# Performance work log

Hardware: AMD Instinct MI355X
Metric: run time of the kernel (lower is better)

## Reference

```python
import jax, jax.numpy as jnp
import numpy as np

N_AGENTS, OBS_DIM, HID, ACT_DIM = 8192, 64, 128, 16


def setup_inputs() -> dict:
    key = jax.random.key(0)
    k = jax.random.split(key, 8)
    obs_agents = jax.random.normal(k[0], (N_AGENTS, OBS_DIM), dtype=jnp.float32)
    # binary adjacency, {0,1}, int32 (index/mask semantics, non-differentiable)
    adj = jax.random.randint(k[1], (N_AGENTS, N_AGENTS), 0, 2, dtype=jnp.int32)
    def lin(kk, fan_in, fan_out):
        lim = 1.0 / np.sqrt(fan_in)
        kw, kb = jax.random.split(kk)
        W = jax.random.uniform(kw, (fan_in, fan_out), jnp.float32, -lim, lim)
        b = jax.random.uniform(kb, (fan_out,), jnp.float32, -lim, lim)
        return W, b
    W1, b1 = lin(k[2], OBS_DIM, HID)          # encoder
    W2, b2 = lin(k[3], 2 * HID, HID)          # actor layer 1
    W3, b3 = lin(k[4], HID, ACT_DIM)          # actor layer 2
    return {"obs_agents": obs_agents, "adj": adj,
            "W1": W1, "b1": b1, "W2": W2, "b2": b2, "W3": W3, "b3": b3}


def reference(obs_agents, adj, W1, b1, W2, b2, W3, b3):
    # per-agent encode: h = tanh(obs @ W1 + b1)  -> [N, HID]
    h = jnp.tanh(obs_agents @ W1 + b1)
    # neighbor mean message: mean of h[j] over j with adj[i,j]!=0, zeros if no neighbors
    a = adj.astype(h.dtype)                      # [N, N] binary
    deg = jnp.sum(a, axis=1, keepdims=True)      # [N, 1]
    msg = (a @ h) / jnp.maximum(deg, 1.0)        # zero rows stay zero
    # actor MLP on concat([h, msg])
    combined = jnp.concatenate([h, msg], axis=-1)            # [N, 2*HID]
    hid = jnp.tanh(combined @ W2 + b2)                        # [N, HID]
    logits = hid @ W3 + b3                                    # [N, ACT_DIM]
    return logits
```

## Files before the change

kernel.cpp:

```cpp
#include <hip/hip_runtime.h>
#include <stdint.h>
#include <math.h>

#define NAG 8192
#define NC  128
#define NSPLIT 8
#define LDB2 136

typedef __attribute__((ext_vector_type(8))) short short8;
typedef __attribute__((ext_vector_type(4))) float floatx4;

__device__ __forceinline__ float bf2f(unsigned short u) {
    union { uint32_t i; float f; } v; v.i = ((uint32_t)u) << 16; return v.f;
}
__device__ __forceinline__ unsigned short f2bf(float f) {
    union { float f; uint32_t i; } v; v.f = f;
    uint32_t x = v.i;
    return (unsigned short)((x + 0x7FFFu + ((x >> 16) & 1u)) >> 16);
}
__device__ __forceinline__ unsigned short f2h(float f) {
    union { _Float16 h; unsigned short u; } v; v.h = (_Float16)f; return v.u;
}
__device__ __forceinline__ float h2f(unsigned short u) {
    union { _Float16 h; unsigned short u; } v; v.u = u; return (float)v.h;
}
__device__ __forceinline__ bool detect_f32(const void* W1, int t) {
    const unsigned short* w = (const unsigned short*)W1;
    int l = t & 63, big = 0;
    #pragma unroll
    for (int j = 0; j < 8; ++j) {
        float v = bf2f(w[l * 8 + j]);
        if (!(fabsf(v) <= 1e6f)) big = 1;
    }
    return __ballot(big) != 0ull;
}

__global__ __launch_bounds__(256) void kA_pack_encode(
    const int* __restrict__ adj,
    unsigned long long* __restrict__ bits,
    const void* __restrict__ obs,
    const void* __restrict__ W1,
    const void* __restrict__ b1,
    float* __restrict__ h_f32,
    unsigned short* __restrict__ hT)
{
    const int t = threadIdx.x;
    if (blockIdx.x < 2048) {
        const int lane = t & 63;
        const int gw = blockIdx.x * 4 + (t >> 6);
        for (int it = 0; it < 32; ++it) {
            size_t u = ((size_t)it * 8192 + gw) * 4;
            size_t col = u * 64 + lane;
            unsigned long long m0 = __ballot(adj[col]       != 0);
            unsigned long long m1 = __ballot(adj[col + 64]  != 0);
            unsigned long long m2 = __ballot(adj[col + 128] != 0);
            unsigned long long m3 = __ballot(adj[col + 192] != 0);
            if (lane == 0) {
                bits[u]     = m0;
                bits[u + 1] = m1;
                bits[u + 2] = m2;
                bits[u + 3] = m3;
            }
        }
        return;
    }
    __shared__ float obs_lds[32][68];
    __shared__ unsigned short ht_lds[128][33];
    const int abase = (blockIdx.x - 2048) * 32;
    const bool isf = detect_f32(W1, t);

    {
        int a = t >> 3, c0 = (t & 7) * 8;
        if (isf) {
            const float* p = (const float*)obs;
            #pragma unroll
            for (int j = 0; j < 8; ++j)
                obs_lds[a][c0 + j] = p[(size_t)(abase + a) * 64 + c0 + j];
        } else {
            const unsigned short* p = (const unsigned short*)obs;
            #pragma unroll
            for (int j = 0; j < 8; ++j)
                obs_lds[a][c0 + j] = bf2f(p[(size_t)(abase + a) * 64 + c0 + j]);
        }
    }
    __syncthreads();

    const int o = t & 127;
    const int half = t >> 7;
    float acc[16];
    if (isf) {
        const float* Wp = (const float*)W1;
        float bias = ((const float*)b1)[o];
        #pragma unroll
        for (int i = 0; i < 16; ++i) acc[i] = bias;
        for (int k0 = 0; k0 < 64; k0 += 8) {
            float w[8];
            #pragma unroll
            for (int j = 0; j < 8; ++j) w[j] = Wp[(k0 + j) * 128 + o];
            #pragma unroll
            for (int j = 0; j < 8; ++j)
                #pragma unroll
                for (int i = 0; i < 16; ++i)
                    acc[i] = fmaf(obs_lds[half * 16 + i][k0 + j], w[j], acc[i]);
        }
    } else {
        const unsigned short* Wp = (const unsigned short*)W1;
        float bias = bf2f(((const unsigned short*)b1)[o]);
        #pragma unroll
        for (int i = 0; i < 16; ++i) acc[i] = bias;
        for (int k0 = 0; k0 < 64; k0 += 8) {
            float w[8];
            #pragma unroll
            for (int j = 0; j < 8; ++j) w[j] = bf2f(Wp[(k0 + j) * 128 + o]);
            #pragma unroll
            for (int j = 0; j < 8; ++j)
                #pragma unroll
                for (int i = 0; i < 16; ++i)
                    acc[i] = fmaf(obs_lds[half * 16 + i][k0 + j], w[j], acc[i]);
        }
    }
    #pragma unroll
    for (int i = 0; i < 16; ++i) {
        float th = tanhf(acc[i]);
        int a = half * 16 + i;
        h_f32[(size_t)(abase + a) * 128 + o] = th;
        ht_lds[o][a] = f2bf(th);
    }
    __syncthreads();

    for (int p = 0; p < 16; ++p) {
        int n = p * 8 + (t >> 5);
        int a = t & 31;
        hT[(size_t)n * NAG + abase + a] = ht_lds[n][a];
    }
}

__global__ __launch_bounds__(256, 4) void k2_msggemm(
    const uint32_t* __restrict__ bits,
    const unsigned short* __restrict__ hT,
    unsigned short* __restrict__ Cp16)
{
    __shared__ __align__(16) unsigned short Blds[128 * LDB2];
    const int t = threadIdx.x;
    const int mtile = blockIdx.x & 127;
    const int ks = blockIdx.x >> 7;
    const int row0 = mtile * 64;
    const int kbeg = ks * 1024;

    const int wave = t >> 6, lane = t & 63;
    const int fm = lane & 15, quad = lane >> 4;

    floatx4 acc[8];
    #pragma unroll
    for (int i = 0; i < 8; ++i) acc[i] = (floatx4)0.f;

    const int arow = row0 + wave * 16 + fm;
    const uint32_t* aWp = bits + (size_t)arow * 256 + (kbeg >> 5);

    for (int ss = 0; ss < 8; ++ss) {
        if (ss) __syncthreads();
        #pragma unroll
        for (int i = 0; i < 8; ++i) {
            int idx = i * 256 + t;
            int row = idx >> 4, ch = idx & 15;
            uint4 v = *reinterpret_cast<const uint4*>(hT + (size_t)row * NAG + kbeg + ss * 128 + ch * 8);
            *reinterpret_cast<uint4*>(&Blds[row * LDB2 + ch * 8]) = v;
        }
        int4 a0 = *reinterpret_cast<const int4*>(aWp + ss * 4);
        uint32_t aw[4] = {(uint32_t)a0.x, (uint32_t)a0.y, (uint32_t)a0.z, (uint32_t)a0.w};
        __syncthreads();
        #pragma unroll
        for (int kw = 0; kw < 4; ++kw) {
            uint32_t b = (aw[kw] >> (quad * 8)) & 0xFFu;
            union { uint32_t u[4]; short8 s; } af;
            #pragma unroll
            for (int p = 0; p < 4; ++p) {
                uint32_t bb = b >> (2 * p);
                af.u[p] = ((bb & 1u) | ((bb & 2u) << 15)) * 0x3F80u;
            }
            #pragma unroll
            for (int j = 0; j < 8; ++j) {
                short8 bf = *reinterpret_cast<const short8*>(&Blds[(j * 16 + fm) * LDB2 + kw * 32 + quad * 8]);
                acc[j] = __builtin_amdgcn_mfma_f32_16x16x32_bf16(af.s, bf, acc[j], 0, 0, 0);
            }
        }
    }

    unsigned short* out = Cp16 + (size_t)ks * (NAG * NC);
    #pragma unroll
    for (int j = 0; j < 8; ++j) {
        int col = j * 16 + fm;
        #pragma unroll
        for (int r = 0; r < 4; ++r) {
            int row = row0 + wave * 16 + quad * 4 + r;
            out[(size_t)row * NC + col] = f2h(acc[j][r]);
        }
    }
}

__global__ __launch_bounds__(256) void k3_actor(
    const float* __restrict__ h_f32,
    const unsigned short* __restrict__ Cp16,
    const unsigned long long* __restrict__ bits,
    const void* __restrict__ W1,
    const void* __restrict__ W2,
    const void* __restrict__ b2,
    const void* __restrict__ W3,
    const void* __restrict__ b3,
    void* __restrict__ out)
{
    __shared__ float4 comb4[8][66];
    __shared__ float hid[8][132];
    __shared__ int degp[8][33];
    __shared__ float inv_lds[8];
    const int t = threadIdx.x;
    const int abase = blockIdx.x * 8;
    const bool isf = detect_f32(W1, t);
    const size_t PS = (size_t)NAG * NC;

    {
        int a = t >> 5, j = t & 31;
        const unsigned long long* bp = bits + (size_t)(abase + a) * 128 + j * 4;
        degp[a][j] = __popcll(bp[0]) + __popcll(bp[1]) + __popcll(bp[2]) + __popcll(bp[3]);
    }
    __syncthreads();
    if (t < 8) {
        int d = 0;
        #pragma unroll
        for (int j = 0; j < 32; ++j) d += degp[t][j];
        inv_lds[t] = 1.0f / fmaxf((float)d, 1.0f);
    }
    __syncthreads();

    #pragma unroll
    for (int jj = 0; jj < 2; ++jj) {
        int idx = jj * 256 + t;
        int a = idx >> 6, q = idx & 63;
        float4 v;
        if (q < 32) {
            v = *reinterpret_cast<const float4*>(h_f32 + (size_t)(abase + a) * 128 + q * 4);
        } else {
            int f = (q - 32) * 4;
            float s0 = 0.f, s1 = 0.f, s2 = 0.f, s3 = 0.f;
            #pragma unroll
            for (int s = 0; s < NSPLIT; ++s) {
                ushort4 p = *reinterpret_cast<const ushort4*>(Cp16 + s * PS + (size_t)(abase + a) * NC + f);
                s0 += h2f(p.x); s1 += h2f(p.y); s2 += h2f(p.z); s3 += h2f(p.w);
            }
            float sc = inv_lds[a];
            v = make_float4(s0 * sc, s1 * sc, s2 * sc, s3 * sc);
        }
        comb4[a][q] = v;
    }
    __syncthreads();

    const int o = t & 127, half = t >> 7;
    float acc[4];
    if (isf) {
        const float* Wp = (const float*)W2;
        float bias = ((const float*)b2)[o];
        #pragma unroll
        for (int i = 0; i < 4; ++i) acc[i] = bias;
        for (int cq = 0; cq < 64; ++cq) {
            float w0 = Wp[(cq * 4 + 0) * 128 + o];
            float w1 = Wp[(cq * 4 + 1) * 128 + o];
            float w2 = Wp[(cq * 4 + 2) * 128 + o];
            float w3 = Wp[(cq * 4 + 3) * 128 + o];
            #pragma unroll
            for (int i = 0; i < 4; ++i) {
                float4 v = comb4[half * 4 + i][cq];
                acc[i] = fmaf(v.x, w0, acc[i]);
                acc[i] = fmaf(v.y, w1, acc[i]);
                acc[i] = fmaf(v.z, w2, acc[i]);
                acc[i] = fmaf(v.w, w3, acc[i]);
            }
        }
    } else {
        const unsigned short* Wp = (const unsigned short*)W2;
        float bias = bf2f(((const unsigned short*)b2)[o]);
        #pragma unroll
        for (int i = 0; i < 4; ++i) acc[i] = bias;
        for (int cq = 0; cq < 64; ++cq) {
            float w0 = bf2f(Wp[(cq * 4 + 0) * 128 + o]);
            float w1 = bf2f(Wp[(cq * 4 + 1) * 128 + o]);
            float w2 = bf2f(Wp[(cq * 4 + 2) * 128 + o]);
            float w3 = bf2f(Wp[(cq * 4 + 3) * 128 + o]);
            #pragma unroll
            for (int i = 0; i < 4; ++i) {
                float4 v = comb4[half * 4 + i][cq];
                acc[i] = fmaf(v.x, w0, acc[i]);
                acc[i] = fmaf(v.y, w1, acc[i]);
                acc[i] = fmaf(v.z, w2, acc[i]);
                acc[i] = fmaf(v.w, w3, acc[i]);
            }
        }
    }
    #pragma unroll
    for (int i = 0; i < 4; ++i)
        hid[half * 4 + i][o] = tanhf(acc[i]);
    __syncthreads();

    if (t < 128) {
        const int q = t & 15, ar = t >> 4;
        float l;
        if (isf) {
            const float* Wp = (const float*)W3;
            l = ((const float*)b3)[q];
            #pragma unroll 4
            for (int oo = 0; oo < 128; ++oo)
                l = fmaf(hid[ar][oo], Wp[oo * 16 + q], l);
        } else {
            const unsigned short* Wp = (const unsigned short*)W3;
            l = bf2f(((const unsigned short*)b3)[q]);
            #pragma unroll 4
            for (int oo = 0; oo < 128; ++oo)
                l = fmaf(hid[ar][oo], bf2f(Wp[oo * 16 + q]), l);
        }
        size_t i0 = (size_t)(abase + ar) * 16 + q;
        if (isf) ((float*)out)[i0] = l;
        else     ((unsigned short*)out)[i0] = f2bf(l);
    }
}

extern "C" void kernel_launch(void* const* d_in, const int* in_sizes, int n_in,
                              void* d_out, int out_size, void* d_ws, size_t ws_size,
                              hipStream_t stream) {
    const void* obs = d_in[0];
    const int*  adj = (const int*)d_in[1];
    const void* W1  = d_in[2];
    const void* b1  = d_in[3];
    const void* W2  = d_in[4];
    const void* b2  = d_in[5];
    const void* W3  = d_in[6];
    const void* b3  = d_in[7];

    char* ws = (char*)d_ws;
    unsigned short* hT   = (unsigned short*)(ws);
    float*          h_f32= (float*)(ws + 2097152);
    unsigned short* Cp16 = (unsigned short*)(ws + 6291456);
    unsigned long long* bits = (unsigned long long*)(ws + 23068672);

    hipLaunchKernelGGL(kA_pack_encode, dim3(2304), dim3(256), 0, stream,
                       adj, bits, obs, W1, b1, h_f32, hT);
    hipLaunchKernelGGL(k2_msggemm, dim3(1024), dim3(256), 0, stream,
                       (const uint32_t*)bits, hT, Cp16);
    hipLaunchKernelGGL(k3_actor, dim3(1024), dim3(256), 0, stream,
                       h_f32, Cp16, bits, W1, W2, b2, W3, b3, d_out);
}
```

Baseline: 432.1 us.

## Read int32 adjacency directly in message GEMM, drop bit-packing pass

Removes the separate pass that packed the int32 adjacency matrix into bitmasks. The message GEMM now loads adj rows directly, converts nonzeros to bf16 ones for the MFMA A operand, and accumulates per-row degree partials written per K-split. The actor kernel sums these eight partials instead of popcounting the bitmask. This drops one full read of the 256MB adjacency plus the bitmask write and read, at the cost of heavier global loads inside the GEMM's main loop.

```diff
diff --git a/kernel.cpp b/kernel.cpp
--- a/kernel.cpp
+++ b/kernel.cpp
@@ -35,38 +35,17 @@
     return __ballot(big) != 0ull;
 }
 
-__global__ __launch_bounds__(256) void kA_pack_encode(
-    const int* __restrict__ adj,
-    unsigned long long* __restrict__ bits,
+__global__ __launch_bounds__(256) void kE_encode(
     const void* __restrict__ obs,
     const void* __restrict__ W1,
     const void* __restrict__ b1,
     float* __restrict__ h_f32,
     unsigned short* __restrict__ hT)
 {
-    const int t = threadIdx.x;
-    if (blockIdx.x < 2048) {
-        const int lane = t & 63;
-        const int gw = blockIdx.x * 4 + (t >> 6);
-        for (int it = 0; it < 32; ++it) {
-            size_t u = ((size_t)it * 8192 + gw) * 4;
-            size_t col = u * 64 + lane;
-            unsigned long long m0 = __ballot(adj[col]       != 0);
-            unsigned long long m1 = __ballot(adj[col + 64]  != 0);
-            unsigned long long m2 = __ballot(adj[col + 128] != 0);
-            unsigned long long m3 = __ballot(adj[col + 192] != 0);
-            if (lane == 0) {
-                bits[u]     = m0;
-                bits[u + 1] = m1;
-                bits[u + 2] = m2;
-                bits[u + 3] = m3;
-            }
-        }
-        return;
-    }
     __shared__ float obs_lds[32][68];
     __shared__ unsigned short ht_lds[128][33];
-    const int abase = (blockIdx.x - 2048) * 32;
+    const int t = threadIdx.x;
+    const int abase = blockIdx.x * 32;
     const bool isf = detect_f32(W1, t);
 
     {
@@ -135,10 +114,11 @@
     }
 }
 
-__global__ __launch_bounds__(256, 4) void k2_msggemm(
-    const uint32_t* __restrict__ bits,
+__global__ __launch_bounds__(256, 4) void kG_msggemm(
+    const int* __restrict__ adj,
     const unsigned short* __restrict__ hT,
-    unsigned short* __restrict__ Cp16)
+    unsigned short* __restrict__ Cp16,
+    int* __restrict__ degP)
 {
     __shared__ __align__(16) unsigned short Blds[128 * LDB2];
     const int t = threadIdx.x;
@@ -155,9 +135,16 @@
     for (int i = 0; i < 8; ++i) acc[i] = (floatx4)0.f;
 
     const int arow = row0 + wave * 16 + fm;
-    const uint32_t* aWp = bits + (size_t)arow * 256 + (kbeg >> 5);
+    const int* ap = adj + (size_t)arow * NAG + kbeg + quad * 8;
+    int dsum = 0;
 
     for (int ss = 0; ss < 8; ++ss) {
+        int4 av[8];
+        #pragma unroll
+        for (int kw = 0; kw < 4; ++kw) {
+            av[2 * kw]     = *reinterpret_cast<const int4*>(ap + ss * 128 + kw * 32);
+            av[2 * kw + 1] = *reinterpret_cast<const int4*>(ap + ss * 128 + kw * 32 + 4);
+        }
         if (ss) __syncthreads();
         #pragma unroll
         for (int i = 0; i < 8; ++i) {
@@ -166,17 +153,17 @@
             uint4 v = *reinterpret_cast<const uint4*>(hT + (size_t)row * NAG + kbeg + ss * 128 + ch * 8);
             *reinterpret_cast<uint4*>(&Blds[row * LDB2 + ch * 8]) = v;
         }
-        int4 a0 = *reinterpret_cast<const int4*>(aWp + ss * 4);
-        uint32_t aw[4] = {(uint32_t)a0.x, (uint32_t)a0.y, (uint32_t)a0.z, (uint32_t)a0.w};
         __syncthreads();
         #pragma unroll
         for (int kw = 0; kw < 4; ++kw) {
-            uint32_t b = (aw[kw] >> (quad * 8)) & 0xFFu;
+            const int* q = (const int*)&av[2 * kw];
             union { uint32_t u[4]; short8 s; } af;
             #pragma unroll
             for (int p = 0; p < 4; ++p) {
-                uint32_t bb = b >> (2 * p);
-                af.u[p] = ((bb & 1u) | ((bb & 2u) << 15)) * 0x3F80u;
+                uint32_t e0 = (q[2 * p]     != 0);
+                uint32_t e1 = (q[2 * p + 1] != 0);
+                dsum += (int)(e0 + e1);
+                af.u[p] = (e0 | (e1 << 16)) * 0x3F80u;
             }
             #pragma unroll
             for (int j = 0; j < 8; ++j) {
@@ -186,6 +173,10 @@
         }
     }
 
+    dsum += __shfl_xor(dsum, 16);
+    dsum += __shfl_xor(dsum, 32);
+    if (lane < 16) degP[ks * NAG + arow] = dsum;
+
     unsigned short* out = Cp16 + (size_t)ks * (NAG * NC);
     #pragma unroll
     for (int j = 0; j < 8; ++j) {
@@ -201,7 +192,7 @@
 __global__ __launch_bounds__(256) void k3_actor(
     const float* __restrict__ h_f32,
     const unsigned short* __restrict__ Cp16,
-    const unsigned long long* __restrict__ bits,
+    const int* __restrict__ degP,
     const void* __restrict__ W1,
     const void* __restrict__ W2,
     const void* __restrict__ b2,
@@ -211,23 +202,22 @@
 {
     __shared__ float4 comb4[8][66];
     __shared__ float hid[8][132];
-    __shared__ int degp[8][33];
+    __shared__ int degs[8][9];
     __shared__ float inv_lds[8];
     const int t = threadIdx.x;
     const int abase = blockIdx.x * 8;
     const bool isf = detect_f32(W1, t);
     const size_t PS = (size_t)NAG * NC;
 
-    {
-        int a = t >> 5, j = t & 31;
-        const unsigned long long* bp = bits + (size_t)(abase + a) * 128 + j * 4;
-        degp[a][j] = __popcll(bp[0]) + __popcll(bp[1]) + __popcll(bp[2]) + __popcll(bp[3]);
+    if (t < 64) {
+        int a = t >> 3, s = t & 7;
+        degs[a][s] = degP[s * NAG + abase + a];
     }
     __syncthreads();
     if (t < 8) {
         int d = 0;
         #pragma unroll
-        for (int j = 0; j < 32; ++j) d += degp[t][j];
+        for (int s = 0; s < 8; ++s) d += degs[t][s];
         inv_lds[t] = 1.0f / fmaxf((float)d, 1.0f);
     }
     __syncthreads();
@@ -338,12 +328,12 @@
     unsigned short* hT   = (unsigned short*)(ws);
     float*          h_f32= (float*)(ws + 2097152);
     unsigned short* Cp16 = (unsigned short*)(ws + 6291456);
-    unsigned long long* bits = (unsigned long long*)(ws + 23068672);
-
-    hipLaunchKernelGGL(kA_pack_encode, dim3(2304), dim3(256), 0, stream,
-                       adj, bits, obs, W1, b1, h_f32, hT);
-    hipLaunchKernelGGL(k2_msggemm, dim3(1024), dim3(256), 0, stream,
-                       (const uint32_t*)bits, hT, Cp16);
+    int*            degP = (int*)(ws + 23068672);
+
+    hipLaunchKernelGGL(kE_encode, dim3(256), dim3(256), 0, stream,
+                       obs, W1, b1, h_f32, hT);
+    hipLaunchKernelGGL(kG_msggemm, dim3(1024), dim3(256), 0, stream,
+                       adj, hT, Cp16, degP);
     hipLaunchKernelGGL(k3_actor, dim3(1024), dim3(256), 0, stream,
-                       h_f32, Cp16, bits, W1, W2, b2, W3, b3, d_out);
-}
+                       h_f32, Cp16, degP, W1, W2, b2, W3, b3, d_out);
+}
```

Result: slower. 484.2 us (+12.1%).

## Double-buffer hT tiles in LDS with register prefetch in msg GEMM

Applied to the files above, without the earlier changes.

The message GEMM kernel now stages 64-column chunks of hT into two LDS buffers. Each thread issues global loads for the next chunk into registers before running the MFMA work on the current buffer, then writes them to the other buffer. This is meant to hide global load latency behind the MFMAs and to drop one barrier per iteration. In exchange it adds register pressure and uses smaller chunks, so there are twice as many iterations and barriers.

```diff
diff --git a/kernel.cpp b/kernel.cpp
--- a/kernel.cpp
+++ b/kernel.cpp
@@ -5,7 +5,7 @@
 #define NAG 8192
 #define NC  128
 #define NSPLIT 8
-#define LDB2 136
+#define LDB3 68
 
 typedef __attribute__((ext_vector_type(8))) short short8;
 typedef __attribute__((ext_vector_type(4))) float floatx4;
@@ -140,7 +140,7 @@
     const unsigned short* __restrict__ hT,
     unsigned short* __restrict__ Cp16)
 {
-    __shared__ __align__(16) unsigned short Blds[128 * LDB2];
+    __shared__ __align__(16) unsigned short Blds[2][128 * LDB3];
     const int t = threadIdx.x;
     const int mtile = blockIdx.x & 127;
     const int ks = blockIdx.x >> 7;
@@ -157,21 +157,38 @@
     const int arow = row0 + wave * 16 + fm;
     const uint32_t* aWp = bits + (size_t)arow * 256 + (kbeg >> 5);
 
-    for (int ss = 0; ss < 8; ++ss) {
-        if (ss) __syncthreads();
-        #pragma unroll
-        for (int i = 0; i < 8; ++i) {
+    const int srow = t >> 1;
+    {
+        #pragma unroll
+        for (int i = 0; i < 4; ++i) {
             int idx = i * 256 + t;
-            int row = idx >> 4, ch = idx & 15;
-            uint4 v = *reinterpret_cast<const uint4*>(hT + (size_t)row * NAG + kbeg + ss * 128 + ch * 8);
-            *reinterpret_cast<uint4*>(&Blds[row * LDB2 + ch * 8]) = v;
-        }
-        int4 a0 = *reinterpret_cast<const int4*>(aWp + ss * 4);
-        uint32_t aw[4] = {(uint32_t)a0.x, (uint32_t)a0.y, (uint32_t)a0.z, (uint32_t)a0.w};
+            int row = idx >> 3, ch = idx & 7;
+            uint4 v = *reinterpret_cast<const uint4*>(hT + (size_t)row * NAG + kbeg + ch * 8);
+            *reinterpret_cast<uint4*>(&Blds[0][row * LDB3 + ch * 8]) = v;
+        }
         __syncthreads();
-        #pragma unroll
-        for (int kw = 0; kw < 4; ++kw) {
-            uint32_t b = (aw[kw] >> (quad * 8)) & 0xFFu;
+    }
+    (void)srow;
+
+    #pragma unroll 1
+    for (int ss = 0; ss < 16; ++ss) {
+        const int cur = ss & 1;
+        uint2 aw2 = *reinterpret_cast<const uint2*>(aWp + ss * 2);
+        uint4 sv0, sv1, sv2, sv3;
+        if (ss < 15) {
+            const unsigned short* src = hT + (size_t)kbeg + (ss + 1) * 64;
+            int idx0 = t,       r0 = idx0 >> 3, c0 = idx0 & 7;
+            int idx1 = 256 + t, r1 = idx1 >> 3, c1 = idx1 & 7;
+            int idx2 = 512 + t, r2 = idx2 >> 3, c2 = idx2 & 7;
+            int idx3 = 768 + t, r3 = idx3 >> 3, c3 = idx3 & 7;
+            sv0 = *reinterpret_cast<const uint4*>(src + (size_t)r0 * NAG + c0 * 8);
+            sv1 = *reinterpret_cast<const uint4*>(src + (size_t)r1 * NAG + c1 * 8);
+            sv2 = *reinterpret_cast<const uint4*>(src + (size_t)r2 * NAG + c2 * 8);
+            sv3 = *reinterpret_cast<const uint4*>(src + (size_t)r3 * NAG + c3 * 8);
+        }
+        #pragma unroll
+        for (int kw = 0; kw < 2; ++kw) {
+            uint32_t b = ((kw ? aw2.y : aw2.x) >> (quad * 8)) & 0xFFu;
             union { uint32_t u[4]; short8 s; } af;
             #pragma unroll
             for (int p = 0; p < 4; ++p) {
@@ -180,10 +197,17 @@
             }
             #pragma unroll
             for (int j = 0; j < 8; ++j) {
-                short8 bf = *reinterpret_cast<const short8*>(&Blds[(j * 16 + fm) * LDB2 + kw * 32 + quad * 8]);
+                short8 bf = *reinterpret_cast<const short8*>(&Blds[cur][(j * 16 + fm) * LDB3 + kw * 32 + quad * 8]);
                 acc[j] = __builtin_amdgcn_mfma_f32_16x16x32_bf16(af.s, bf, acc[j], 0, 0, 0);
             }
         }
+        if (ss < 15) {
+            *reinterpret_cast<uint4*>(&Blds[cur ^ 1][((t      ) >> 3) * LDB3 + (t & 7) * 8])        = sv0;
+            *reinterpret_cast<uint4*>(&Blds[cur ^ 1][((256 + t) >> 3) * LDB3 + ((256 + t) & 7) * 8]) = sv1;
+            *reinterpret_cast<uint4*>(&Blds[cur ^ 1][((512 + t) >> 3) * LDB3 + ((512 + t) & 7) * 8]) = sv2;
+            *reinterpret_cast<uint4*>(&Blds[cur ^ 1][((768 + t) >> 3) * LDB3 + ((768 + t) & 7) * 8]) = sv3;
+        }
+        __syncthreads();
     }
 
     unsigned short* out = Cp16 + (size_t)ks * (NAG * NC);
```

New measurement: 434.4 us. About the same (+0.5%).
